# Kernel optimization log

Measured on AMD Instinct MI355X. Metric: run time of the kernel, lower is better.

The kernel has to match this reference:

```python
import jax, jax.numpy as jnp
import numpy as np
from jax import lax

B, CH, OUT = 2, 128, 128
H, W = 64, 64
S = 2            # scale_factor
K = 5            # up_kernel
COMP = 64        # compressed_channels
EK = 3           # encoder_kernel
K2 = K * K


def setup_inputs() -> dict:
    key = jax.random.key(0)
    ks = jax.random.split(key, 4)
    x = jax.random.normal(ks[0], (B, CH, H, W), jnp.float32)
    w_comp = jax.random.normal(ks[1], (COMP, CH), jnp.float32) * 0.05
    b_comp = jnp.zeros((COMP,), jnp.float32)
    # content encoder init std=0.001 (per normal_init in the source)
    w_enc = jax.random.normal(ks[2], (K2 * S * S, COMP, EK, EK), jnp.float32) * 0.001
    b_enc = jnp.zeros((K2 * S * S,), jnp.float32)
    w_proj = jax.random.normal(ks[3], (OUT, CH), jnp.float32) * 0.05
    b_proj = jnp.zeros((OUT,), jnp.float32)
    return {"x": x, "w_comp": w_comp, "b_comp": b_comp,
            "w_enc": w_enc, "b_enc": b_enc,
            "w_proj": w_proj, "b_proj": b_proj}


def _conv1x1(x, w, b):
    # x: (B,C,H,W), w: (O,C) -> (B,O,H,W)
    return jnp.einsum('bchw,oc->bohw', x, w) + b[None, :, None, None]


def reference(x, w_comp, b_comp, w_enc, b_enc, w_proj, b_proj):
    n, c, h, w = x.shape
    # 1) channel compressor (1x1 conv)
    compressed = _conv1x1(x, w_comp, b_comp)
    # 2) content encoder (3x3 conv, padding 1)
    kernel = lax.conv_general_dilated(
        compressed, w_enc, window_strides=(1, 1), padding=[(1, 1), (1, 1)],
        dimension_numbers=('NCHW', 'OIHW', 'NCHW')) + b_enc[None, :, None, None]
    # 3) kernel normalizer: pixel_shuffle(S) then softmax over k^2 positions
    # (B, K2*S*S, h, w) -> (B, K2, h*S, w*S)
    kernel = kernel.reshape(n, K2, S, S, h, w)
    kernel = kernel.transpose(0, 1, 4, 2, 5, 3).reshape(n, K2, h * S, w * S)
    kernel = jax.nn.softmax(kernel, axis=1)
    # 4) feature reassembly
    Hs, Ws = h * S, w * S
    x_up = jnp.repeat(jnp.repeat(x, S, axis=2), S, axis=3)   # nearest upsample
    p = (K // 2) * S                                         # unfold padding
    xp = jnp.pad(x_up, ((0, 0), (0, 0), (p, p), (p, p)))
    # unfold with kernel K, dilation S -> (B, C, K2, Hs, Ws), (kh, kw) row-major
    patches = jnp.stack(
        [xp[:, :, i * S:i * S + Hs, j * S:j * S + Ws]
         for i in range(K) for j in range(K)], axis=2)
    out = jnp.einsum('bkhw,bckhw->bchw', kernel, patches)
    # 5) projection (1x1 conv)
    return _conv1x1(out, w_proj, b_proj)
```

## Files before the change

kernel.cpp:

```cpp
#include <hip/hip_runtime.h>

constexpr int QQ = 100;

using short8 = __attribute__((ext_vector_type(8))) short;
using f32x4  = __attribute__((ext_vector_type(4))) float;

__device__ inline unsigned short f2bf(float f) {
    unsigned u = __float_as_uint(f);
    return (unsigned short)((u + 0x7FFF + ((u >> 16) & 1)) >> 16);
}
__device__ inline float bf2f(unsigned short us) {
    return __uint_as_float(((unsigned)us) << 16);
}

__global__ __launch_bounds__(256)
void k_prep(const float* __restrict__ x, const float* __restrict__ we,
            const float* __restrict__ wc, const float* __restrict__ be,
            const float* __restrict__ bc, const float* __restrict__ wproj,
            unsigned short* __restrict__ xt, unsigned short* __restrict__ weff,
            float* __restrict__ beff, unsigned short* __restrict__ wpb) {
    int blk = blockIdx.x;
    int tid = threadIdx.x;
    if (blk < 128) {
        __shared__ unsigned short t[64 * 136];
        int b = blk >> 6, y = blk & 63;
        int lx = tid & 63, cg = tid >> 6;
        const float* xb = x + (b * 128 + cg * 32) * 4096 + y * 64 + lx;
#pragma unroll 8
        for (int i = 0; i < 32; ++i)
            t[lx * 136 + cg * 32 + i] = f2bf(xb[i * 4096]);
        __syncthreads();
        int px = tid >> 2, ck = tid & 3;
        unsigned short* dst = xt + (b * 4096 + y * 64 + px) * 128 + ck * 32;
        const unsigned short* src = t + px * 136 + ck * 32;
#pragma unroll
        for (int j = 0; j < 4; ++j)
            *(short8*)(dst + j * 8) = *(const short8*)(src + j * 8);
        return;
    }
    if (blk < 704) {
        int gid = (blk - 128) * 256 + tid;
        int q = gid / 1152;
        int r = gid - q * 1152;
        float acc = 0.f;
        if (q < QQ) {
            const float* wep = we + q * 576 + (r >> 7);
            const float* wcp = wc + (r & 127);
#pragma unroll 8
            for (int m = 0; m < 64; ++m)
                acc += wep[m * 9] * wcp[m * 128];
        }
        weff[gid] = f2bf(acc);
        return;
    }
    if (tid < 128) {
        float s = 0.f;
        if (tid < QQ) {
            s = be[tid];
            for (int m = 0; m < 64; ++m) {
                float t2 = 0.f;
#pragma unroll
                for (int k = 0; k < 9; ++k) t2 += we[(tid * 64 + m) * 9 + k];
                s += t2 * bc[m];
            }
        }
        beff[tid] = s;
    }
    for (int i = tid; i < 16384; i += 256)
        wpb[i] = f2bf(wproj[i]);
}

__global__ __launch_bounds__(256)
void k_enc(const unsigned short* __restrict__ xt, const unsigned short* __restrict__ weff,
           float* __restrict__ P) {
    __shared__ unsigned short xhs[100 * 136];
    int blk = blockIdx.x;
    int ks = blk >> 7;
    int rem = blk & 127;
    int b = rem >> 6;
    int tile = rem & 63;
    int y0 = (tile >> 3) * 8, x0 = (tile & 7) * 8;
    int tid = threadIdx.x;
    int lane = tid & 63, w = tid >> 6;
    int l15 = lane & 15, kgrp = lane >> 4;

    short8 afr[3][4][2];
#pragma unroll
    for (int kk = 0; kk < 3; ++kk)
#pragma unroll
        for (int cs = 0; cs < 4; ++cs)
#pragma unroll
            for (int mf = 0; mf < 2; ++mf) {
                int q = (w * 2 + mf) * 16 + l15;
                afr[kk][cs][mf] = *(const short8*)(weff + (q * 9 + ks * 3 + kk) * 128
                                                   + cs * 32 + kgrp * 8);
            }

    for (int idx = tid; idx < 800; idx += 256) {
        int hp = idx >> 3, cq = idx & 7;
        int hy = hp / 10, hx = hp - hy * 10;
        int gy = y0 - 1 + hy, gx = x0 - 1 + hx;
        short8 v0 = {0,0,0,0,0,0,0,0}, v1 = {0,0,0,0,0,0,0,0};
        if ((unsigned)gy < 64u && (unsigned)gx < 64u) {
            const unsigned short* src = xt + (b * 4096 + gy * 64 + gx) * 128 + cq * 16;
            v0 = *(const short8*)src;
            v1 = *(const short8*)(src + 8);
        }
        *(short8*)&xhs[hp * 136 + cq * 16] = v0;
        *(short8*)&xhs[hp * 136 + cq * 16 + 8] = v1;
    }
    __syncthreads();

    int px = 0;
    f32x4 acc[2][4];
#pragma unroll
    for (int mf = 0; mf < 2; ++mf)
#pragma unroll
        for (int nf = 0; nf < 4; ++nf) acc[mf][nf] = f32x4{0.f, 0.f, 0.f, 0.f};

#pragma unroll
    for (int kk = 0; kk < 3; ++kk) {
        int kap = ks * 3 + kk;
        int dy = kap / 3, dx = kap % 3;
#pragma unroll
        for (int nf = 0; nf < 4; ++nf) {
            px = nf * 16 + l15;
            int py = px >> 3, pxx = px & 7;
            int hp = (py + dy) * 10 + (pxx + dx);
#pragma unroll
            for (int cs = 0; cs < 4; ++cs) {
                short8 bfrag = *(const short8*)&xhs[hp * 136 + cs * 32 + kgrp * 8];
#pragma unroll
                for (int mf = 0; mf < 2; ++mf)
                    acc[mf][nf] = __builtin_amdgcn_mfma_f32_16x16x32_bf16(
                        afr[kk][cs][mf], bfrag, acc[mf][nf], 0, 0, 0);
            }
        }
    }
    float* Pb = P + (ks * 2 + b) * QQ * 4096;
#pragma unroll
    for (int mf = 0; mf < 2; ++mf)
#pragma unroll
        for (int nf = 0; nf < 4; ++nf) {
            px = nf * 16 + l15;
            int py = px >> 3, pxx = px & 7;
            int gpx = (y0 + py) * 64 + (x0 + pxx);
            int qb = (w * 2 + mf) * 16 + kgrp * 4;
#pragma unroll
            for (int r = 0; r < 4; ++r)
                if (qb + r < QQ) Pb[(qb + r) * 4096 + gpx] = acc[mf][nf][r];
        }
}

__global__ __launch_bounds__(256)
void k_re(const unsigned short* __restrict__ xt, const float* __restrict__ P,
          const float* __restrict__ beff, unsigned short* __restrict__ re) {
    __shared__ unsigned short xs[72 * 136];
    __shared__ float sm[1600];
    int bid = blockIdx.x;
    int b = bid >> 8;
    int rem = bid & 255;
    int ty = rem >> 3, tx = rem & 7;
    int tid = threadIdx.x;

    int R0 = ty * 2 - 2, C0 = tx * 8 - 2;
    for (int idx = tid; idx < 576; idx += 256) {
        int hp = idx >> 3, cq = idx & 7;
        int hy = hp / 12, hx = hp - hy * 12;
        int gr = R0 + hy, gc = C0 + hx;
        short8 v0 = {0,0,0,0,0,0,0,0}, v1 = {0,0,0,0,0,0,0,0};
        if ((unsigned)gr < 64u && (unsigned)gc < 64u) {
            const unsigned short* src = xt + (b * 4096 + gr * 64 + gc) * 128 + cq * 16;
            v0 = *(const short8*)src;
            v1 = *(const short8*)(src + 8);
        }
        *(short8*)&xs[hp * 136 + cq * 16] = v0;
        *(short8*)&xs[hp * 136 + cq * 16 + 8] = v1;
    }
    for (int idx = tid; idx < 1600; idx += 256) {
        int q = idx >> 4, lowpx = idx & 15;
        int h0 = ty * 2 + (lowpx >> 3), w0 = tx * 8 + (lowpx & 7);
        int px = (h0 << 6) + w0;
        float v = P[(b * QQ + q) * 4096 + px]
                + P[((2 + b) * QQ + q) * 4096 + px]
                + P[((4 + b) * QQ + q) * 4096 + px] + beff[q];
        sm[(q >> 2) * 64 + lowpx * 4 + (q & 3)] = v;
    }
    __syncthreads();
    {
        int e = tid >> 2, kg = tid & 3;
        float v[7];
        float m = -1e30f;
#pragma unroll
        for (int j = 0; j < 7; ++j) {
            int k = kg + 4 * j;
            float val = (k < 25) ? sm[k * 64 + e] : -1e30f;
            v[j] = val; m = fmaxf(m, val);
        }
        m = fmaxf(m, __shfl_xor(m, 1));
        m = fmaxf(m, __shfl_xor(m, 2));
        float s = 0.f;
#pragma unroll
        for (int j = 0; j < 7; ++j) {
            int k = kg + 4 * j;
            if (k < 25) { v[j] = __expf(v[j] - m); s += v[j]; }
        }
        s += __shfl_xor(s, 1);
        s += __shfl_xor(s, 2);
        float inv = 1.f / s;
#pragma unroll
        for (int j = 0; j < 7; ++j) {
            int k = kg + 4 * j;
            if (k < 25) sm[k * 64 + e] = v[j] * inv;
        }
    }
    __syncthreads();
    int lowpx = tid & 15, cgrp = tid >> 4;
    int ly = lowpx >> 3, lx = lowpx & 7;
    float acc[8][4];
#pragma unroll
    for (int cc = 0; cc < 8; ++cc)
#pragma unroll
        for (int s = 0; s < 4; ++s) acc[cc][s] = 0.f;
#pragma unroll
    for (int k = 0; k < 25; ++k) {
        int i = k / 5, j = k % 5;
        float4 wk4 = *(const float4*)&sm[k * 64 + lowpx * 4];
        short8 tap8 = *(const short8*)&xs[((ly + i) * 12 + (lx + j)) * 136 + cgrp * 8];
#pragma unroll
        for (int cc = 0; cc < 8; ++cc) {
            float tap = bf2f((unsigned short)tap8[cc]);
            acc[cc][0] += wk4.x * tap;
            acc[cc][1] += wk4.y * tap;
            acc[cc][2] += wk4.z * tap;
            acc[cc][3] += wk4.w * tap;
        }
    }
    int hb = ty * 4 + ly * 2, wb = tx * 16 + lx * 2;
#pragma unroll
    for (int s = 0; s < 4; ++s) {
        int hs = hb + (s >> 1), ws = wb + (s & 1);
        short8 pk;
#pragma unroll
        for (int cc = 0; cc < 8; ++cc) pk[cc] = (short)f2bf(acc[cc][s]);
        *(short8*)(re + (b * 16384 + hs * 128 + ws) * 128 + cgrp * 8) = pk;
    }
}

__global__ __launch_bounds__(256)
void k_proj(const unsigned short* __restrict__ re, const unsigned short* __restrict__ wpb,
            const float* __restrict__ bproj, float* __restrict__ out) {
    __shared__ unsigned short At[128 * 136];
    __shared__ unsigned short Bt[64 * 136];
    __shared__ float bs[128];
    int blk = blockIdx.x;
    int b = blk >> 8;
    int pbase = (blk & 255) * 64;
    int tid = threadIdx.x;
    for (int idx = tid; idx < 1024; idx += 256) {
        int o = idx >> 3, cq = idx & 7;
        const unsigned short* s = wpb + o * 128 + cq * 16;
        *(short8*)&At[o * 136 + cq * 16]     = *(const short8*)s;
        *(short8*)&At[o * 136 + cq * 16 + 8] = *(const short8*)(s + 8);
    }
    for (int idx = tid; idx < 512; idx += 256) {
        int p = idx >> 3, cq = idx & 7;
        const unsigned short* s = re + (b * 16384 + pbase + p) * 128 + cq * 16;
        *(short8*)&Bt[p * 136 + cq * 16]     = *(const short8*)s;
        *(short8*)&Bt[p * 136 + cq * 16 + 8] = *(const short8*)(s + 8);
    }
    if (tid < 128) bs[tid] = bproj[tid];
    __syncthreads();
    int lane = tid & 63, w = tid >> 6;
    int l15 = lane & 15, kgrp = lane >> 4;
    f32x4 acc[8];
#pragma unroll
    for (int mf = 0; mf < 8; ++mf) acc[mf] = f32x4{0.f, 0.f, 0.f, 0.f};
#pragma unroll
    for (int cs = 0; cs < 4; ++cs) {
        short8 bfrag = *(const short8*)&Bt[(w * 16 + l15) * 136 + cs * 32 + kgrp * 8];
#pragma unroll
        for (int mf = 0; mf < 8; ++mf) {
            short8 af = *(const short8*)&At[(mf * 16 + l15) * 136 + cs * 32 + kgrp * 8];
            acc[mf] = __builtin_amdgcn_mfma_f32_16x16x32_bf16(af, bfrag, acc[mf], 0, 0, 0);
        }
    }
    int p = pbase + w * 16 + l15;
    float* ob = out + (b * 128) * 16384 + p;
#pragma unroll
    for (int mf = 0; mf < 8; ++mf) {
        int qb = mf * 16 + kgrp * 4;
#pragma unroll
        for (int r = 0; r < 4; ++r)
            ob[(qb + r) * 16384] = acc[mf][r] + bs[qb + r], ob += 0;
    }
}

extern "C" void kernel_launch(void* const* d_in, const int* in_sizes, int n_in,
                              void* d_out, int out_size, void* d_ws, size_t ws_size,
                              hipStream_t stream) {
    const float* x      = (const float*)d_in[0];
    const float* w_comp = (const float*)d_in[1];
    const float* b_comp = (const float*)d_in[2];
    const float* w_enc  = (const float*)d_in[3];
    const float* b_enc  = (const float*)d_in[4];
    const float* w_proj = (const float*)d_in[5];
    const float* b_proj = (const float*)d_in[6];
    float* out = (float*)d_out;

    char* base = (char*)d_ws;
    unsigned short* xt   = (unsigned short*)(base);
    unsigned short* weff = (unsigned short*)(base + 2097152);
    float*          beff = (float*)         (base + 2392064);
    unsigned short* wpb  = (unsigned short*)(base + 2392576);
    float*          P    = (float*)         (base + 2425344);
    unsigned short* re   = (unsigned short*)(base + 12255744);

    k_prep<<<705, 256, 0, stream>>>(x, w_enc, w_comp, b_enc, b_comp, w_proj,
                                    xt, weff, beff, wpb);
    k_enc<<<384, 256, 0, stream>>>(xt, weff, P);
    k_re<<<512, 256, 0, stream>>>(xt, P, beff, re);
    k_proj<<<512, 256, 0, stream>>>(re, wpb, b_proj, out);
}
```

Before: 122.7 us.

## Fuse encoder conv, reassembly and projection into one kernel with MFMA-ready weight layouts

```diff
diff --git a/kernel.cpp b/kernel.cpp
--- a/kernel.cpp
+++ b/kernel.cpp
@@ -17,40 +17,52 @@
 void k_prep(const float* __restrict__ x, const float* __restrict__ we,
             const float* __restrict__ wc, const float* __restrict__ be,
             const float* __restrict__ bc, const float* __restrict__ wproj,
-            unsigned short* __restrict__ xt, unsigned short* __restrict__ weff,
-            float* __restrict__ beff, unsigned short* __restrict__ wpb) {
-    int blk = blockIdx.x;
-    int tid = threadIdx.x;
-    if (blk < 128) {
-        __shared__ unsigned short t[64 * 136];
-        int b = blk >> 6, y = blk & 63;
+            unsigned short* __restrict__ xt, unsigned short* __restrict__ weffR,
+            float* __restrict__ beff, unsigned short* __restrict__ wpbR) {
+    __shared__ float smf[2880];
+    int blk = blockIdx.x, tid = threadIdx.x;
+    if (blk < 512) {
+        unsigned short* t = (unsigned short*)smf;
+        int b = blk >> 8, y = (blk >> 2) & 63, cq = blk & 3;
         int lx = tid & 63, cg = tid >> 6;
-        const float* xb = x + (b * 128 + cg * 32) * 4096 + y * 64 + lx;
-#pragma unroll 8
-        for (int i = 0; i < 32; ++i)
-            t[lx * 136 + cg * 32 + i] = f2bf(xb[i * 4096]);
+        const float* xb = x + (b * 128 + cq * 32 + cg * 8) * 4096 + y * 64 + lx;
+#pragma unroll
+        for (int i = 0; i < 8; ++i)
+            t[lx * 40 + cg * 8 + i] = f2bf(xb[i * 4096]);
         __syncthreads();
-        int px = tid >> 2, ck = tid & 3;
-        unsigned short* dst = xt + (b * 4096 + y * 64 + px) * 128 + ck * 32;
-        const unsigned short* src = t + px * 136 + ck * 32;
-#pragma unroll
-        for (int j = 0; j < 4; ++j)
-            *(short8*)(dst + j * 8) = *(const short8*)(src + j * 8);
+        int px = tid >> 2, j = tid & 3;
+        *(short8*)(xt + (b * 4096 + y * 64 + px) * 128 + cq * 32 + j * 8)
+            = *(const short8*)(t + px * 40 + j * 8);
         return;
     }
-    if (blk < 704) {
-        int gid = (blk - 128) * 256 + tid;
-        int q = gid / 1152;
-        int r = gid - q * 1152;
-        float acc = 0.f;
+    if (blk < 624) {
+        int q = blk - 512;
+        float* we_s = smf;
+        float* red  = smf + 576;
         if (q < QQ) {
-            const float* wep = we + q * 576 + (r >> 7);
-            const float* wcp = wc + (r & 127);
-#pragma unroll 8
-            for (int m = 0; m < 64; ++m)
-                acc += wep[m * 9] * wcp[m * 128];
-        }
-        weff[gid] = f2bf(acc);
+            for (int idx = tid; idx < 576; idx += 256) we_s[idx] = we[q * 576 + idx];
+            __syncthreads();
+            int c = tid & 127, mh = tid >> 7;
+            float acc[9];
+#pragma unroll
+            for (int k = 0; k < 9; ++k) acc[k] = 0.f;
+            for (int m = 0; m < 32; ++m) {
+                int mm = mh * 32 + m;
+                float wv = wc[mm * 128 + c];
+#pragma unroll
+                for (int k = 0; k < 9; ++k) acc[k] += we_s[mm * 9 + k] * wv;
+            }
+#pragma unroll
+            for (int k = 0; k < 9; ++k) red[(mh * 9 + k) * 128 + c] = acc[k];
+            __syncthreads();
+        }
+        int mf = q >> 4, l15 = q & 15;
+        for (int idx = tid; idx < 1152; idx += 256) {
+            int kap = idx >> 7, r = idx & 127;
+            float v = (q < QQ) ? (red[kap * 128 + r] + red[(9 + kap) * 128 + r]) : 0.f;
+            int c32 = r >> 5, kgrp = (r >> 3) & 3, j = r & 7;
+            weffR[(((kap * 4 + c32) * 7 + mf) * 64 + kgrp * 16 + l15) * 8 + j] = f2bf(v);
+        }
         return;
     }
     if (tid < 128) {
@@ -66,102 +78,30 @@
         }
         beff[tid] = s;
     }
-    for (int i = tid; i < 16384; i += 256)
-        wpb[i] = f2bf(wproj[i]);
+    for (int idx = tid; idx < 16384; idx += 256) {
+        int o = idx >> 7, c = idx & 127;
+        int cs = c >> 5, kgrp = (c >> 3) & 3, j = c & 7;
+        int mf = o >> 4, l15 = o & 15;
+        wpbR[((cs * 8 + mf) * 64 + kgrp * 16 + l15) * 8 + j] = f2bf(wproj[idx]);
+    }
 }
 
 __global__ __launch_bounds__(256)
-void k_enc(const unsigned short* __restrict__ xt, const unsigned short* __restrict__ weff,
-           float* __restrict__ P) {
-    __shared__ unsigned short xhs[100 * 136];
-    int blk = blockIdx.x;
-    int ks = blk >> 7;
-    int rem = blk & 127;
-    int b = rem >> 6;
-    int tile = rem & 63;
-    int y0 = (tile >> 3) * 8, x0 = (tile & 7) * 8;
+void k_main(const unsigned short* __restrict__ xt, const unsigned short* __restrict__ weffR,
+            const float* __restrict__ beff, const unsigned short* __restrict__ wpbR,
+            const float* __restrict__ bproj, float* __restrict__ out) {
+    __shared__ __align__(16) char smem[56448];
+    unsigned short* xs = (unsigned short*)smem;
+    float* sm          = (float*)(smem + 19584);
+    float* psum        = (float*)(smem + 25984);
+    unsigned short* re = (unsigned short*)(smem + 25984);
+
+    int bid = blockIdx.x;
+    int b = bid >> 8, rem = bid & 255;
+    int ty = rem >> 3, tx = rem & 7;
     int tid = threadIdx.x;
     int lane = tid & 63, w = tid >> 6;
     int l15 = lane & 15, kgrp = lane >> 4;
-
-    short8 afr[3][4][2];
-#pragma unroll
-    for (int kk = 0; kk < 3; ++kk)
-#pragma unroll
-        for (int cs = 0; cs < 4; ++cs)
-#pragma unroll
-            for (int mf = 0; mf < 2; ++mf) {
-                int q = (w * 2 + mf) * 16 + l15;
-                afr[kk][cs][mf] = *(const short8*)(weff + (q * 9 + ks * 3 + kk) * 128
-                                                   + cs * 32 + kgrp * 8);
-            }
-
-    for (int idx = tid; idx < 800; idx += 256) {
-        int hp = idx >> 3, cq = idx & 7;
-        int hy = hp / 10, hx = hp - hy * 10;
-        int gy = y0 - 1 + hy, gx = x0 - 1 + hx;
-        short8 v0 = {0,0,0,0,0,0,0,0}, v1 = {0,0,0,0,0,0,0,0};
-        if ((unsigned)gy < 64u && (unsigned)gx < 64u) {
-            const unsigned short* src = xt + (b * 4096 + gy * 64 + gx) * 128 + cq * 16;
-            v0 = *(const short8*)src;
-            v1 = *(const short8*)(src + 8);
-        }
-        *(short8*)&xhs[hp * 136 + cq * 16] = v0;
-        *(short8*)&xhs[hp * 136 + cq * 16 + 8] = v1;
-    }
-    __syncthreads();
-
-    int px = 0;
-    f32x4 acc[2][4];
-#pragma unroll
-    for (int mf = 0; mf < 2; ++mf)
-#pragma unroll
-        for (int nf = 0; nf < 4; ++nf) acc[mf][nf] = f32x4{0.f, 0.f, 0.f, 0.f};
-
-#pragma unroll
-    for (int kk = 0; kk < 3; ++kk) {
-        int kap = ks * 3 + kk;
-        int dy = kap / 3, dx = kap % 3;
-#pragma unroll
-        for (int nf = 0; nf < 4; ++nf) {
-            px = nf * 16 + l15;
-            int py = px >> 3, pxx = px & 7;
-            int hp = (py + dy) * 10 + (pxx + dx);
-#pragma unroll
-            for (int cs = 0; cs < 4; ++cs) {
-                short8 bfrag = *(const short8*)&xhs[hp * 136 + cs * 32 + kgrp * 8];
-#pragma unroll
-                for (int mf = 0; mf < 2; ++mf)
-                    acc[mf][nf] = __builtin_amdgcn_mfma_f32_16x16x32_bf16(
-                        afr[kk][cs][mf], bfrag, acc[mf][nf], 0, 0, 0);
-            }
-        }
-    }
-    float* Pb = P + (ks * 2 + b) * QQ * 4096;
-#pragma unroll
-    for (int mf = 0; mf < 2; ++mf)
-#pragma unroll
-        for (int nf = 0; nf < 4; ++nf) {
-            px = nf * 16 + l15;
-            int py = px >> 3, pxx = px & 7;
-            int gpx = (y0 + py) * 64 + (x0 + pxx);
-            int qb = (w * 2 + mf) * 16 + kgrp * 4;
-#pragma unroll
-            for (int r = 0; r < 4; ++r)
-                if (qb + r < QQ) Pb[(qb + r) * 4096 + gpx] = acc[mf][nf][r];
-        }
-}
-
-__global__ __launch_bounds__(256)
-void k_re(const unsigned short* __restrict__ xt, const float* __restrict__ P,
-          const float* __restrict__ beff, unsigned short* __restrict__ re) {
-    __shared__ unsigned short xs[72 * 136];
-    __shared__ float sm[1600];
-    int bid = blockIdx.x;
-    int b = bid >> 8;
-    int rem = bid & 255;
-    int ty = rem >> 3, tx = rem & 7;
-    int tid = threadIdx.x;
 
     int R0 = ty * 2 - 2, C0 = tx * 8 - 2;
     for (int idx = tid; idx < 576; idx += 256) {
@@ -174,19 +114,44 @@
             v0 = *(const short8*)src;
             v1 = *(const short8*)(src + 8);
         }
-        *(short8*)&xs[hp * 136 + cq * 16] = v0;
+        *(short8*)&xs[hp * 136 + cq * 16]     = v0;
         *(short8*)&xs[hp * 136 + cq * 16 + 8] = v1;
     }
+    __syncthreads();
+
+    int ly = l15 >> 3, lx = l15 & 7;
+    f32x4 acc[7];
+#pragma unroll
+    for (int mf = 0; mf < 7; ++mf) acc[mf] = f32x4{0.f, 0.f, 0.f, 0.f};
+#pragma unroll
+    for (int kap = 0; kap < 9; ++kap) {
+        int dy = kap / 3, dx = kap % 3;
+        short8 bfrag = *(const short8*)&xs[((ly + dy + 1) * 12 + lx + dx + 1) * 136
+                                           + w * 32 + kgrp * 8];
+        const unsigned short* wrk = weffR + ((kap * 4 + w) * 7) * 512 + lane * 8;
+#pragma unroll
+        for (int mf = 0; mf < 7; ++mf) {
+            short8 af = *(const short8*)(wrk + mf * 512);
+            acc[mf] = __builtin_amdgcn_mfma_f32_16x16x32_bf16(af, bfrag, acc[mf], 0, 0, 0);
+        }
+    }
+#pragma unroll
+    for (int mf = 0; mf < 7; ++mf)
+#pragma unroll
+        for (int r = 0; r < 4; ++r) {
+            int q = mf * 16 + kgrp * 4 + r;
+            psum[(w * 112 + q) * 17 + l15] = acc[mf][r];
+        }
+    __syncthreads();
+
     for (int idx = tid; idx < 1600; idx += 256) {
         int q = idx >> 4, lowpx = idx & 15;
-        int h0 = ty * 2 + (lowpx >> 3), w0 = tx * 8 + (lowpx & 7);
-        int px = (h0 << 6) + w0;
-        float v = P[(b * QQ + q) * 4096 + px]
-                + P[((2 + b) * QQ + q) * 4096 + px]
-                + P[((4 + b) * QQ + q) * 4096 + px] + beff[q];
+        float v = psum[q * 17 + lowpx] + psum[(112 + q) * 17 + lowpx]
+                + psum[(224 + q) * 17 + lowpx] + psum[(336 + q) * 17 + lowpx] + beff[q];
         sm[(q >> 2) * 64 + lowpx * 4 + (q & 3)] = v;
     }
     __syncthreads();
+
     {
         int e = tid >> 2, kg = tid & 3;
         float v[7];
@@ -215,85 +180,62 @@
         }
     }
     __syncthreads();
-    int lowpx = tid & 15, cgrp = tid >> 4;
-    int ly = lowpx >> 3, lx = lowpx & 7;
-    float acc[8][4];
-#pragma unroll
-    for (int cc = 0; cc < 8; ++cc)
-#pragma unroll
-        for (int s = 0; s < 4; ++s) acc[cc][s] = 0.f;
-#pragma unroll
-    for (int k = 0; k < 25; ++k) {
-        int i = k / 5, j = k % 5;
-        float4 wk4 = *(const float4*)&sm[k * 64 + lowpx * 4];
-        short8 tap8 = *(const short8*)&xs[((ly + i) * 12 + (lx + j)) * 136 + cgrp * 8];
-#pragma unroll
-        for (int cc = 0; cc < 8; ++cc) {
-            float tap = bf2f((unsigned short)tap8[cc]);
-            acc[cc][0] += wk4.x * tap;
-            acc[cc][1] += wk4.y * tap;
-            acc[cc][2] += wk4.z * tap;
-            acc[cc][3] += wk4.w * tap;
-        }
-    }
-    int hb = ty * 4 + ly * 2, wb = tx * 16 + lx * 2;
-#pragma unroll
-    for (int s = 0; s < 4; ++s) {
-        int hs = hb + (s >> 1), ws = wb + (s & 1);
-        short8 pk;
-#pragma unroll
-        for (int cc = 0; cc < 8; ++cc) pk[cc] = (short)f2bf(acc[cc][s]);
-        *(short8*)(re + (b * 16384 + hs * 128 + ws) * 128 + cgrp * 8) = pk;
-    }
-}
-
-__global__ __launch_bounds__(256)
-void k_proj(const unsigned short* __restrict__ re, const unsigned short* __restrict__ wpb,
-            const float* __restrict__ bproj, float* __restrict__ out) {
-    __shared__ unsigned short At[128 * 136];
-    __shared__ unsigned short Bt[64 * 136];
-    __shared__ float bs[128];
-    int blk = blockIdx.x;
-    int b = blk >> 8;
-    int pbase = (blk & 255) * 64;
-    int tid = threadIdx.x;
-    for (int idx = tid; idx < 1024; idx += 256) {
-        int o = idx >> 3, cq = idx & 7;
-        const unsigned short* s = wpb + o * 128 + cq * 16;
-        *(short8*)&At[o * 136 + cq * 16]     = *(const short8*)s;
-        *(short8*)&At[o * 136 + cq * 16 + 8] = *(const short8*)(s + 8);
-    }
-    for (int idx = tid; idx < 512; idx += 256) {
-        int p = idx >> 3, cq = idx & 7;
-        const unsigned short* s = re + (b * 16384 + pbase + p) * 128 + cq * 16;
-        *(short8*)&Bt[p * 136 + cq * 16]     = *(const short8*)s;
-        *(short8*)&Bt[p * 136 + cq * 16 + 8] = *(const short8*)(s + 8);
-    }
-    if (tid < 128) bs[tid] = bproj[tid];
-    __syncthreads();
-    int lane = tid & 63, w = tid >> 6;
-    int l15 = lane & 15, kgrp = lane >> 4;
-    f32x4 acc[8];
-#pragma unroll
-    for (int mf = 0; mf < 8; ++mf) acc[mf] = f32x4{0.f, 0.f, 0.f, 0.f};
+
+    {
+        int lowpx = tid & 15, cgrp = tid >> 4;
+        int ly2 = lowpx >> 3, lx2 = lowpx & 7;
+        float racc[8][4];
+#pragma unroll
+        for (int cc = 0; cc < 8; ++cc)
+#pragma unroll
+            for (int s = 0; s < 4; ++s) racc[cc][s] = 0.f;
+#pragma unroll
+        for (int k = 0; k < 25; ++k) {
+            int i = k / 5, j = k % 5;
+            float4 wk4 = *(const float4*)&sm[k * 64 + lowpx * 4];
+            short8 tap8 = *(const short8*)&xs[((ly2 + i) * 12 + (lx2 + j)) * 136 + cgrp * 8];
+#pragma unroll
+            for (int cc = 0; cc < 8; ++cc) {
+                float tap = bf2f((unsigned short)tap8[cc]);
+                racc[cc][0] += wk4.x * tap;
+                racc[cc][1] += wk4.y * tap;
+                racc[cc][2] += wk4.z * tap;
+                racc[cc][3] += wk4.w * tap;
+            }
+        }
+#pragma unroll
+        for (int s = 0; s < 4; ++s) {
+            int p = (ly2 * 2 + (s >> 1)) * 16 + lx2 * 2 + (s & 1);
+            short8 pk;
+#pragma unroll
+            for (int cc = 0; cc < 8; ++cc) pk[cc] = (short)f2bf(racc[cc][s]);
+            *(short8*)&re[p * 136 + cgrp * 8] = pk;
+        }
+    }
+    __syncthreads();
+
+    f32x4 pacc[8];
+#pragma unroll
+    for (int mf = 0; mf < 8; ++mf) pacc[mf] = f32x4{0.f, 0.f, 0.f, 0.f};
 #pragma unroll
     for (int cs = 0; cs < 4; ++cs) {
-        short8 bfrag = *(const short8*)&Bt[(w * 16 + l15) * 136 + cs * 32 + kgrp * 8];
+        short8 bfrag = *(const short8*)&re[(w * 16 + l15) * 136 + cs * 32 + kgrp * 8];
+        const unsigned short* wrp = wpbR + (cs * 8) * 512 + lane * 8;
 #pragma unroll
         for (int mf = 0; mf < 8; ++mf) {
-            short8 af = *(const short8*)&At[(mf * 16 + l15) * 136 + cs * 32 + kgrp * 8];
-            acc[mf] = __builtin_amdgcn_mfma_f32_16x16x32_bf16(af, bfrag, acc[mf], 0, 0, 0);
-        }
-    }
-    int p = pbase + w * 16 + l15;
-    float* ob = out + (b * 128) * 16384 + p;
-#pragma unroll
-    for (int mf = 0; mf < 8; ++mf) {
-        int qb = mf * 16 + kgrp * 4;
-#pragma unroll
-        for (int r = 0; r < 4; ++r)
-            ob[(qb + r) * 16384] = acc[mf][r] + bs[qb + r], ob += 0;
-    }
+            short8 af = *(const short8*)(wrp + mf * 512);
+            pacc[mf] = __builtin_amdgcn_mfma_f32_16x16x32_bf16(af, bfrag, pacc[mf], 0, 0, 0);
+        }
+    }
+    int hs = ty * 4 + w, ws = tx * 16 + l15;
+    float* ob = out + (b * 128) * 16384 + hs * 128 + ws;
+#pragma unroll
+    for (int mf = 0; mf < 8; ++mf)
+#pragma unroll
+        for (int r = 0; r < 4; ++r) {
+            int o = mf * 16 + kgrp * 4 + r;
+            ob[o * 16384] = pacc[mf][r] + bproj[o];
+        }
 }
 
 extern "C" void kernel_launch(void* const* d_in, const int* in_sizes, int n_in,
@@ -309,16 +251,12 @@
     float* out = (float*)d_out;
 
     char* base = (char*)d_ws;
-    unsigned short* xt   = (unsigned short*)(base);
-    unsigned short* weff = (unsigned short*)(base + 2097152);
-    float*          beff = (float*)         (base + 2392064);
-    unsigned short* wpb  = (unsigned short*)(base + 2392576);
-    float*          P    = (float*)         (base + 2425344);
-    unsigned short* re   = (unsigned short*)(base + 12255744);
-
-    k_prep<<<705, 256, 0, stream>>>(x, w_enc, w_comp, b_enc, b_comp, w_proj,
-                                    xt, weff, beff, wpb);
-    k_enc<<<384, 256, 0, stream>>>(xt, weff, P);
-    k_re<<<512, 256, 0, stream>>>(xt, P, beff, re);
-    k_proj<<<512, 256, 0, stream>>>(re, wpb, b_proj, out);
-}
+    unsigned short* xt    = (unsigned short*)(base);
+    unsigned short* weffR = (unsigned short*)(base + 2097152);
+    float*          beff  = (float*)         (base + 2355200);
+    unsigned short* wpbR  = (unsigned short*)(base + 2355712);
+
+    k_prep<<<625, 256, 0, stream>>>(x, w_enc, w_comp, b_enc, b_comp, w_proj,
+                                    xt, weffR, beff, wpbR);
+    k_main<<<512, 256, 0, stream>>>(xt, weffR, beff, wpbR, b_proj, out);
+}
```

New measurement: 106.8 us. 1.15x faster.
